# Performance work log

Measured on AMD Instinct MI355X. Metric: run time of the kernel, lower is better.

The kernel has to match this reference:

```python
import jax, jax.numpy as jnp
import numpy as np

N_NODES = 100000


def _gcn_layer(x, W, b, row, col, ew, n):
    # PyG GCNConv: x' = D^{-1/2} (A + I) D^{-1/2} (x W) + b
    xw = x @ W  # [N, out]
    deg = jax.ops.segment_sum(ew, col, num_segments=n)  # weighted in-degree incl. self loops
    dinv = jnp.where(deg > 0, jax.lax.rsqrt(deg), 0.0)
    norm = dinv[row] * ew * dinv[col]  # [E]
    msg = xw[row] * norm[:, None]  # [E, out] gather + scale
    out = jax.ops.segment_sum(msg, col, num_segments=n) + b
    return out


def setup_inputs() -> dict:
    key = jax.random.key(0)
    k = jax.random.split(key, 6)
    E = 1600000
    h = 64
    x = jax.random.normal(k[0], (N_NODES, 4), dtype=jnp.float32)
    edge_index = jax.random.randint(k[1], (2, E), 0, N_NODES, dtype=jnp.int64)
    edge_weight = jax.random.uniform(k[2], (E,), dtype=jnp.float32)
    W1 = jax.random.normal(k[3], (4, h), dtype=jnp.float32) * (1.0 / np.sqrt(4))
    b1 = jnp.zeros((h,), dtype=jnp.float32)
    W2 = jax.random.normal(k[4], (h, h), dtype=jnp.float32) * (1.0 / np.sqrt(h))
    b2 = jnp.zeros((h,), dtype=jnp.float32)
    return {"x": x, "edge_index": edge_index, "edge_weight": edge_weight,
            "W1": W1, "b1": b1, "W2": W2, "b2": b2}


def reference(x, edge_index, edge_weight, W1, b1, W2, b2):
    n = x.shape[0]
    # add self loops with weight 1 (GCNConv default add_self_loops=True)
    loop = jnp.arange(n, dtype=edge_index.dtype)
    row = jnp.concatenate([edge_index[0], loop])
    col = jnp.concatenate([edge_index[1], loop])
    ew = jnp.concatenate([edge_weight, jnp.ones((n,), dtype=edge_weight.dtype)])
    h = jax.nn.relu(_gcn_layer(x, W1, b1, row, col, ew, n))
    out = jax.nn.relu(_gcn_layer(h, W2, b2, row, col, ew, n))
    return out
```

## Files before the change

### kernel.cpp

```cpp
#include <hip/hip_runtime.h>

#define H 64
#define BKT_SHIFT 7
#define BKT_NODES 128
#define NB 782
#define CAP 2432
#define SC_K 8
#define SC_T 512
#define SC_TILE (SC_K * SC_T)

typedef __attribute__((ext_vector_type(8))) short short8v;
typedef __attribute__((ext_vector_type(4))) float float4v;

__device__ __forceinline__ float bf2f(unsigned short u) {
    return __uint_as_float(((unsigned)u) << 16);
}
__device__ __forceinline__ unsigned short f2bf(float f) {
    unsigned u = __float_as_uint(f);
    unsigned r = ((u >> 16) & 1u) + 0x7FFFu;
    return (unsigned short)((u + r) >> 16);
}
__device__ __forceinline__ float bflo(unsigned d) { return __uint_as_float(d << 16); }
__device__ __forceinline__ float bfhi(unsigned d) { return __uint_as_float(d & 0xFFFF0000u); }


__global__ void k_prep(const float* __restrict__ W2, unsigned short* __restrict__ W2Tb) {
    int g = blockIdx.x * 256 + threadIdx.x;
    if (g < H * H) {
        int c = g >> 6, k = g & 63;
        W2Tb[g] = f2bf(W2[k * H + c]);
    }
}


__global__ __launch_bounds__(SC_T) void k_bscatter(
        const int* __restrict__ row, const int* __restrict__ col,
        const float* __restrict__ ew, unsigned* __restrict__ cursor,
        uint2* __restrict__ sorted, int E) {
    __shared__ unsigned hist[NB];
    __shared__ unsigned gbase[NB];
    int t = threadIdx.x;
    for (int b = t; b < NB; b += SC_T) hist[b] = 0;
    __syncthreads();
    int tile = blockIdx.x * SC_TILE;
    unsigned st[SC_K];
#pragma unroll
    for (int k = 0; k < SC_K; ++k) {
        int e = tile + k * SC_T + t;
        unsigned enc = 0xFFFFFFFFu;
        if (e < E) {
            unsigned c = (unsigned)col[e];
            unsigned b = c >> BKT_SHIFT;
            unsigned nl = c & (BKT_NODES - 1);
            unsigned r = atomicAdd(&hist[b], 1u);
            enc = (b << 20) | (nl << 13) | r;
        }
        st[k] = enc;
    }
    __syncthreads();
    for (int b = t; b < NB; b += SC_T) {
        unsigned h = hist[b];
        if (h) gbase[b] = (unsigned)b * CAP + atomicAdd(&cursor[b], h);
    }
    __syncthreads();
#pragma unroll
    for (int k = 0; k < SC_K; ++k) {
        int e = tile + k * SC_T + t;
        if (e >= E) continue;
        unsigned enc = st[k];
        unsigned b = enc >> 20, nl = (enc >> 13) & 127u, r = enc & 8191u;
        unsigned pk = ((unsigned)row[e] << 7) | nl;
        sorted[gbase[b] + r] = make_uint2(pk, __float_as_uint(ew[e]));
    }
}


__global__ __launch_bounds__(256) void k_bsort(const uint2* __restrict__ sorted,
                                               const unsigned* __restrict__ cursor,
                                               const float* __restrict__ x,
                                               uint2* __restrict__ sorted2,
                                               unsigned* __restrict__ startA,
                                               unsigned* __restrict__ cntA,
                                               float* __restrict__ dinv,
                                               unsigned short* __restrict__ xqb, int n) {
    __shared__ unsigned hist[BKT_NODES];
    __shared__ unsigned base_[BKT_NODES];
    __shared__ float deg[BKT_NODES];
    __shared__ unsigned wsum;
    int b = blockIdx.x, t = threadIdx.x;
    if (t < BKT_NODES) { hist[t] = 0; deg[t] = 1.0f; }
    __syncthreads();
    unsigned s = (unsigned)b * CAP, e = s + cursor[b];
    uint2 st[10];
#pragma unroll
    for (int k = 0; k < 10; ++k) {
        unsigned j = s + (unsigned)t + ((unsigned)k << 8);
        if (j < e) {
            uint2 u = sorted[j];
            st[k] = u;
            unsigned nl = u.x & 127u;
            atomicAdd(&hist[nl], 1u);
            atomicAdd(&deg[nl], __uint_as_float(u.y));
        }
    }
    __syncthreads();
    if (t < BKT_NODES) {
        unsigned v = hist[t];
        unsigned sc = v;
#pragma unroll
        for (int d = 1; d < 64; d <<= 1) {
            unsigned u = __shfl_up(sc, d);
            if ((t & 63) >= d) sc += u;
        }
        if (t == 63) wsum = sc;
        base_[t] = sc - v;
        int node = b * BKT_NODES + t;
        if (node < n) {
            cntA[node] = v;
            float di = rsqrtf(deg[t]);
            dinv[node] = di;
            float4 xv = ((const float4*)x)[node];
            ushort4 o;
            o.x = f2bf(xv.x * di); o.y = f2bf(xv.y * di);
            o.z = f2bf(xv.z * di); o.w = f2bf(xv.w * di);
            ((ushort4*)xqb)[node] = o;
        }
        hist[t] = 0;
    }
    __syncthreads();
    if (t >= 64 && t < BKT_NODES) base_[t] += wsum;
    __syncthreads();
    if (t < BKT_NODES) {
        int node = b * BKT_NODES + t;
        if (node < n) startA[node] = s + base_[t];
    }
    __syncthreads();
#pragma unroll
    for (int k = 0; k < 10; ++k) {
        unsigned j = s + (unsigned)t + ((unsigned)k << 8);
        if (j < e) {
            uint2 u = st[k];
            unsigned nl = u.x & 127u;
            unsigned pos = atomicAdd(&hist[nl], 1u);
            sorted2[s + base_[nl] + pos] = make_uint2(u.x & 0xFFFFFF80u, u.y);
        }
    }
}


__global__ __launch_bounds__(256) void k_agg1(const uint2* __restrict__ sorted2,
                                              const unsigned* __restrict__ startA,
                                              const unsigned* __restrict__ cntA,
                                              const unsigned short* __restrict__ xqb,
                                              float4* __restrict__ agg4, int n) {
    int g = blockIdx.x * 256 + threadIdx.x;
    int node = g >> 1, half = g & 1;
    if (node >= n) return;
    unsigned s0 = startA[node];
    unsigned cnt = cntA[node];
    unsigned cH = cnt >> 1;
    unsigned s = s0 + (half ? cH : 0u);
    unsigned c = half ? (cnt - cH) : cH;
    const char* xq = (const char*)xqb;
    float a0, a1, a2, a3;
    if (half == 0) {
        uint2 sq = *(const uint2*)(xqb + ((size_t)node << 2));
        a0 = bflo(sq.x); a1 = bfhi(sq.x); a2 = bflo(sq.y); a3 = bfhi(sq.y);
    } else {
        a0 = a1 = a2 = a3 = 0.0f;
    }
    unsigned j = 0;
    for (; j + 8 <= c; j += 8) {
        uint2 p[8], q[8];
#pragma unroll
        for (int k = 0; k < 8; ++k) p[k] = sorted2[s + j + k];
#pragma unroll
        for (int k = 0; k < 8; ++k) q[k] = *(const uint2*)(xq + (p[k].x >> 4));
#pragma unroll
        for (int k = 0; k < 8; ++k) {
            float w = __uint_as_float(p[k].y);
            a0 = fmaf(bflo(q[k].x), w, a0); a1 = fmaf(bfhi(q[k].x), w, a1);
            a2 = fmaf(bflo(q[k].y), w, a2); a3 = fmaf(bfhi(q[k].y), w, a3);
        }
    }
    for (; j < c; ++j) {
        uint2 p = sorted2[s + j];
        uint2 q = *(const uint2*)(xq + (p.x >> 4));
        float w = __uint_as_float(p.y);
        a0 = fmaf(bflo(q.x), w, a0); a1 = fmaf(bfhi(q.x), w, a1);
        a2 = fmaf(bflo(q.y), w, a2); a3 = fmaf(bfhi(q.y), w, a3);
    }
    agg4[((size_t)node << 1) + half] = make_float4(a0, a1, a2, a3);
}


__global__ __launch_bounds__(256) void k_l2front(const float4* __restrict__ agg4,
                                                 const float* __restrict__ W1,
                                                 const float* __restrict__ b1,
                                                 const unsigned short* __restrict__ W2Tb,
                                                 const float* __restrict__ dinv,
                                                 unsigned short* __restrict__ xs2b, int n) {
    __shared__ unsigned short ht[64 * H];
    __shared__ unsigned short wt[H * H];
    __shared__ float w1s[4 * H];
    __shared__ float b1s[H];
    int tid = threadIdx.x;
    int base = blockIdx.x * 64;
    w1s[tid] = W1[tid];
    if (tid < H) b1s[tid] = b1[tid];
    for (int idx = tid; idx < 512; idx += 256) {
        int r = idx >> 3, c = idx & 7;
        uint4 v = *(const uint4*)(W2Tb + (r << 6) + (c << 3));
        *(uint4*)(wt + (r << 6) + ((c ^ (r & 7)) << 3)) = v;
    }
    __syncthreads();
    {
        int r = tid >> 2, ch = tid & 3;
        int node = base + r;
        float4 avA = (node < n) ? agg4[(size_t)node << 1] : make_float4(0.f, 0.f, 0.f, 0.f);
        float4 avB = (node < n) ? agg4[((size_t)node << 1) + 1] : make_float4(0.f, 0.f, 0.f, 0.f);
        float4 av = make_float4(avA.x + avB.x, avA.y + avB.y, avA.z + avB.z, avA.w + avB.w);
        float di = (node < n) ? dinv[node] : 0.0f;
#pragma unroll
        for (int cc = 0; cc < 2; ++cc) {
            int cl = ch * 2 + cc;
            uint4 ov;
            unsigned* op = (unsigned*)&ov;
#pragma unroll
            for (int d = 0; d < 4; ++d) {
                int col = (cl << 3) + (d << 1);
                float h0 = av.x * w1s[col]     + av.y * w1s[H + col]
                         + av.z * w1s[2*H+col] + av.w * w1s[3*H + col];
                float h1 = av.x * w1s[col+1]     + av.y * w1s[H + col+1]
                         + av.z * w1s[2*H+col+1] + av.w * w1s[3*H + col+1];
                h0 = fmaxf(di * h0 + b1s[col], 0.0f);
                h1 = fmaxf(di * h1 + b1s[col + 1], 0.0f);
                op[d] = ((unsigned)f2bf(h1) << 16) | f2bf(h0);
            }
            *(uint4*)(ht + (r << 6) + ((cl ^ (r & 7)) << 3)) = ov;
        }
    }
    __syncthreads();
    int lane = tid & 63;
    int wv = tid >> 6;
    int R = wv * 16;
    int lr = lane & 15, lq = lane >> 4;
    short8v a[2], b[4][2];
#pragma unroll
    for (int kk = 0; kk < 2; ++kk) {
        int rowi = R + lr;
        int cl = kk * 4 + lq;
        a[kk] = *(const short8v*)(ht + (rowi << 6) + ((cl ^ (rowi & 7)) << 3));
    }
#pragma unroll
    for (int nt = 0; nt < 4; ++nt)
#pragma unroll
        for (int kk = 0; kk < 2; ++kk) {
            int rowi = nt * 16 + lr;
            int cl = kk * 4 + lq;
            b[nt][kk] = *(const short8v*)(wt + (rowi << 6) + ((cl ^ (rowi & 7)) << 3));
        }
    float4v acc[4] = {};
#pragma unroll
    for (int nt = 0; nt < 4; ++nt)
#pragma unroll
        for (int kk = 0; kk < 2; ++kk)
            acc[nt] = __builtin_amdgcn_mfma_f32_16x16x32_bf16(a[kk], b[nt][kk],
                                                              acc[nt], 0, 0, 0);
#pragma unroll
    for (int i = 0; i < 4; ++i) {
        int node = base + R + lq * 4 + i;
        if (node < n) {
            float di = dinv[node];
#pragma unroll
            for (int nt = 0; nt < 4; ++nt)
                xs2b[((size_t)node << 6) + nt * 16 + lr] = f2bf(acc[nt][i] * di);
        }
    }
}


__global__ __launch_bounds__(256) void k_agg2(const uint2* __restrict__ sorted2,
                                              const unsigned* __restrict__ startA,
                                              const unsigned* __restrict__ cntA,
                                              const float* __restrict__ dinv,
                                              const unsigned short* __restrict__ xsb,
                                              const float* __restrict__ bias,
                                              float* __restrict__ outf, int n) {
    int wv = (int)(__builtin_amdgcn_readfirstlane(threadIdx.x) >> 6);
    int wid = blockIdx.x * 4 + wv;
    if (wid >= n) return;
    int lane = threadIdx.x & 63;
    int eg = lane >> 3;
    int c8 = lane & 7;
    unsigned s = startA[wid];
    unsigned cnt = cntA[wid];
    float di = dinv[wid];
    const char* xb = (const char*)xsb + (c8 << 4);
    float a0=0.f,a1=0.f,a2=0.f,a3=0.f,a4=0.f,a5=0.f,a6=0.f,a7=0.f;
    for (unsigned b = 0; b < cnt; b += 32) {
        unsigned iA = b + (unsigned)eg;
        unsigned iB = iA + 8u, iC = iA + 16u, iD = iA + 24u;
        uint2 pA = sorted2[s + (iA < cnt ? iA : 0u)];
        uint2 pB = sorted2[s + (iB < cnt ? iB : 0u)];
        uint2 pC = sorted2[s + (iC < cnt ? iC : 0u)];
        uint2 pD = sorted2[s + (iD < cnt ? iD : 0u)];
        float wA = iA < cnt ? __uint_as_float(pA.y) : 0.0f;
        float wB = iB < cnt ? __uint_as_float(pB.y) : 0.0f;
        float wC = iC < cnt ? __uint_as_float(pC.y) : 0.0f;
        float wD = iD < cnt ? __uint_as_float(pD.y) : 0.0f;
        uint4 dA = *(const uint4*)(xb + pA.x);
        uint4 dB = *(const uint4*)(xb + pB.x);
        uint4 dC = *(const uint4*)(xb + pC.x);
        uint4 dD = *(const uint4*)(xb + pD.x);
        a0 = fmaf(bflo(dA.x), wA, a0); a1 = fmaf(bfhi(dA.x), wA, a1);
        a2 = fmaf(bflo(dA.y), wA, a2); a3 = fmaf(bfhi(dA.y), wA, a3);
        a4 = fmaf(bflo(dA.z), wA, a4); a5 = fmaf(bfhi(dA.z), wA, a5);
        a6 = fmaf(bflo(dA.w), wA, a6); a7 = fmaf(bfhi(dA.w), wA, a7);
        a0 = fmaf(bflo(dB.x), wB, a0); a1 = fmaf(bfhi(dB.x), wB, a1);
        a2 = fmaf(bflo(dB.y), wB, a2); a3 = fmaf(bfhi(dB.y), wB, a3);
        a4 = fmaf(bflo(dB.z), wB, a4); a5 = fmaf(bfhi(dB.z), wB, a5);
        a6 = fmaf(bflo(dB.w), wB, a6); a7 = fmaf(bfhi(dB.w), wB, a7);
        a0 = fmaf(bflo(dC.x), wC, a0); a1 = fmaf(bfhi(dC.x), wC, a1);
        a2 = fmaf(bflo(dC.y), wC, a2); a3 = fmaf(bfhi(dC.y), wC, a3);
        a4 = fmaf(bflo(dC.z), wC, a4); a5 = fmaf(bfhi(dC.z), wC, a5);
        a6 = fmaf(bflo(dC.w), wC, a6); a7 = fmaf(bfhi(dC.w), wC, a7);
        a0 = fmaf(bflo(dD.x), wD, a0); a1 = fmaf(bfhi(dD.x), wD, a1);
        a2 = fmaf(bflo(dD.y), wD, a2); a3 = fmaf(bfhi(dD.y), wD, a3);
        a4 = fmaf(bflo(dD.z), wD, a4); a5 = fmaf(bfhi(dD.z), wD, a5);
        a6 = fmaf(bflo(dD.w), wD, a6); a7 = fmaf(bfhi(dD.w), wD, a7);
    }
    a0 += __shfl_xor(a0, 8); a0 += __shfl_xor(a0, 16); a0 += __shfl_xor(a0, 32);
    a1 += __shfl_xor(a1, 8); a1 += __shfl_xor(a1, 16); a1 += __shfl_xor(a1, 32);
    a2 += __shfl_xor(a2, 8); a2 += __shfl_xor(a2, 16); a2 += __shfl_xor(a2, 32);
    a3 += __shfl_xor(a3, 8); a3 += __shfl_xor(a3, 16); a3 += __shfl_xor(a3, 32);
    a4 += __shfl_xor(a4, 8); a4 += __shfl_xor(a4, 16); a4 += __shfl_xor(a4, 32);
    a5 += __shfl_xor(a5, 8); a5 += __shfl_xor(a5, 16); a5 += __shfl_xor(a5, 32);
    a6 += __shfl_xor(a6, 8); a6 += __shfl_xor(a6, 16); a6 += __shfl_xor(a6, 32);
    a7 += __shfl_xor(a7, 8); a7 += __shfl_xor(a7, 16); a7 += __shfl_xor(a7, 32);
    uint4 sv = *(const uint4*)((const char*)xsb + (((size_t)(unsigned)wid) << 7) + (c8 << 4));
    a0 += bflo(sv.x); a1 += bfhi(sv.x);
    a2 += bflo(sv.y); a3 += bfhi(sv.y);
    a4 += bflo(sv.z); a5 += bfhi(sv.z);
    a6 += bflo(sv.w); a7 += bfhi(sv.w);
    const float* bp = bias + (c8 << 3);
    float r0 = fmaxf(di * a0 + bp[0], 0.0f);
    float r1 = fmaxf(di * a1 + bp[1], 0.0f);
    float r2 = fmaxf(di * a2 + bp[2], 0.0f);
    float r3 = fmaxf(di * a3 + bp[3], 0.0f);
    float r4 = fmaxf(di * a4 + bp[4], 0.0f);
    float r5 = fmaxf(di * a5 + bp[5], 0.0f);
    float r6 = fmaxf(di * a6 + bp[6], 0.0f);
    float r7 = fmaxf(di * a7 + bp[7], 0.0f);
    if (eg == 0) {
        float4 o = {r0, r1, r2, r3};
        *(float4*)(outf + (((size_t)wid) << 6) + (c8 << 3)) = o;
    } else if (eg == 1) {
        float4 o = {r4, r5, r6, r7};
        *(float4*)(outf + (((size_t)wid) << 6) + (c8 << 3) + 4) = o;
    }
}


extern "C" void kernel_launch(void* const* d_in, const int* in_sizes, int n_in,
                              void* d_out, int out_size, void* d_ws, size_t ws_size,
                              hipStream_t stream) {
    const float* x  = (const float*)d_in[0];
    const int*   ei = (const int*)d_in[1];
    const float* ew = (const float*)d_in[2];
    const float* W1 = (const float*)d_in[3];
    const float* b1 = (const float*)d_in[4];
    const float* W2 = (const float*)d_in[5];
    const float* b2 = (const float*)d_in[6];
    float* out = (float*)d_out;

    const int n = in_sizes[0] / 4;
    const int E = in_sizes[2];
    const int* row = ei;
    const int* col = ei + E;

    char* p = (char*)d_ws;
    unsigned* cursor = (unsigned*)p;            p += 1024 * 4;
    unsigned short* W2Tb = (unsigned short*)p;  p += (size_t)H * H * 2;
    float* dinv      = (float*)p;               p += (size_t)n * 4;
    unsigned* startA = (unsigned*)p;            p += (size_t)n * 4;
    unsigned* cntA   = (unsigned*)p;            p += (size_t)n * 4;
    unsigned short* xqb = (unsigned short*)p;   p += (size_t)n * 4 * 2;
    float4* agg4     = (float4*)p;              p += ((size_t)2 * n + 128) * 16;
    unsigned short* xs2b = (unsigned short*)p;  p += ((size_t)n + 1) * H * 2;
    uint2* sorted    = (uint2*)p;               p += ((size_t)NB * CAP + 64) * 8;
    uint2* sorted2   = (uint2*)p;

    (void)hipMemsetAsync(cursor, 0, 1024 * 4, stream);
    k_prep<<<16, 256, 0, stream>>>(W2, W2Tb);

    k_bscatter<<<(E + SC_TILE - 1) / SC_TILE, SC_T, 0, stream>>>(row, col, ew, cursor, sorted, E);

    k_bsort<<<NB, 256, 0, stream>>>(sorted, cursor, x, sorted2, startA, cntA, dinv, xqb, n);

    k_agg1<<<(2 * n + 255) / 256, 256, 0, stream>>>(sorted2, startA, cntA, xqb, agg4, n);

    k_l2front<<<(n + 63) / 64, 256, 0, stream>>>(agg4, W1, b1, W2Tb, dinv, xs2b, n);

    k_agg2<<<(n + 3) / 4, 256, 0, stream>>>(sorted2, startA, cntA, dinv, xs2b, b2, out, n);
}
```

Before: 125.1 us.

## Split edge bucket scatter into two-pass coarse then fine radix binning

Replaces the single-pass scatter into 782 buckets with two passes. The first pass bins edges into 49 coarse buckets and stores the 4-bit fine bucket id in the low mantissa bits of the edge weight. The second pass splits each coarse bucket into 16 fine buckets. The aim is better write coalescing and fewer global atomics, since each block writes into fewer destinations. The cost is an extra read and write of the edge array, and the weight's low 4 mantissa bits are overwritten, which slightly perturbs precision.

```diff
diff --git a/kernel.cpp b/kernel.cpp
--- a/kernel.cpp
+++ b/kernel.cpp
@@ -5,9 +5,10 @@
 #define BKT_NODES 128
 #define NB 782
 #define CAP 2432
-#define SC_K 8
-#define SC_T 512
-#define SC_TILE (SC_K * SC_T)
+#define NC 49
+#define CAPC 38400
+#define NCHUNK 5
+#define CHB (CAPC / NCHUNK)
 
 typedef __attribute__((ext_vector_type(8))) short short8v;
 typedef __attribute__((ext_vector_type(4))) float float4v;
@@ -33,44 +34,97 @@
 }
 
 
-__global__ __launch_bounds__(SC_T) void k_bscatter(
+__global__ __launch_bounds__(512) void k_binA(
         const int* __restrict__ row, const int* __restrict__ col,
-        const float* __restrict__ ew, unsigned* __restrict__ cursor,
-        uint2* __restrict__ sorted, int E) {
-    __shared__ unsigned hist[NB];
-    __shared__ unsigned gbase[NB];
+        const float* __restrict__ ew, unsigned* __restrict__ cursorC,
+        uint2* __restrict__ coarse, int E) {
+    __shared__ unsigned hist[NC];
+    __shared__ unsigned gbase[NC];
     int t = threadIdx.x;
-    for (int b = t; b < NB; b += SC_T) hist[b] = 0;
-    __syncthreads();
-    int tile = blockIdx.x * SC_TILE;
-    unsigned st[SC_K];
-#pragma unroll
-    for (int k = 0; k < SC_K; ++k) {
-        int e = tile + k * SC_T + t;
+    if (t < NC) hist[t] = 0;
+    __syncthreads();
+    int tile = blockIdx.x * 8192;
+    unsigned st[16];
+#pragma unroll
+    for (int k = 0; k < 16; ++k) {
+        int e = tile + k * 512 + t;
         unsigned enc = 0xFFFFFFFFu;
         if (e < E) {
             unsigned c = (unsigned)col[e];
-            unsigned b = c >> BKT_SHIFT;
-            unsigned nl = c & (BKT_NODES - 1);
-            unsigned r = atomicAdd(&hist[b], 1u);
-            enc = (b << 20) | (nl << 13) | r;
+            unsigned cb = c >> 11;
+            unsigned fl = (c >> 7) & 15u;
+            unsigned nl = c & 127u;
+            unsigned r = atomicAdd(&hist[cb], 1u);
+            enc = (cb << 24) | (fl << 20) | (nl << 13) | r;
         }
         st[k] = enc;
     }
     __syncthreads();
-    for (int b = t; b < NB; b += SC_T) {
-        unsigned h = hist[b];
-        if (h) gbase[b] = (unsigned)b * CAP + atomicAdd(&cursor[b], h);
-    }
-    __syncthreads();
-#pragma unroll
-    for (int k = 0; k < SC_K; ++k) {
-        int e = tile + k * SC_T + t;
+    if (t < NC) {
+        unsigned h = hist[t];
+        if (h) gbase[t] = (unsigned)t * CAPC + atomicAdd(&cursorC[t], h);
+    }
+    __syncthreads();
+#pragma unroll
+    for (int k = 0; k < 16; ++k) {
+        int e = tile + k * 512 + t;
         if (e >= E) continue;
         unsigned enc = st[k];
-        unsigned b = enc >> 20, nl = (enc >> 13) & 127u, r = enc & 8191u;
+        unsigned cb = enc >> 24, fl = (enc >> 20) & 15u;
+        unsigned nl = (enc >> 13) & 127u, r = enc & 8191u;
         unsigned pk = ((unsigned)row[e] << 7) | nl;
-        sorted[gbase[b] + r] = make_uint2(pk, __float_as_uint(ew[e]));
+        unsigned wb = (__float_as_uint(ew[e]) & 0xFFFFFFF0u) | fl;
+        coarse[gbase[cb] + r] = make_uint2(pk, wb);
+    }
+}
+
+
+__global__ __launch_bounds__(512) void k_binB(
+        const uint2* __restrict__ coarse, const unsigned* __restrict__ cursorC,
+        unsigned* __restrict__ cursorF, uint2* __restrict__ sorted) {
+    __shared__ unsigned hist4[4][16];
+    __shared__ unsigned gbase4[4][16];
+    int t = threadIdx.x;
+    int c = blockIdx.x / NCHUNK;
+    int ch = blockIdx.x % NCHUNK;
+    int grp = t >> 7;
+    if (t < 64) ((unsigned*)hist4)[t] = 0;
+    __syncthreads();
+    int cntC = (int)cursorC[c];
+    int base0 = c * CAPC + ch * CHB;
+    int m = cntC - ch * CHB; if (m > CHB) m = CHB; if (m < 0) m = 0;
+    unsigned st[15];
+#pragma unroll
+    for (int k = 0; k < 15; ++k) {
+        int i = t + k * 512;
+        unsigned enc = 0xFFFFFFFFu;
+        if (i < m) {
+            unsigned fl = coarse[base0 + i].y & 15u;
+            unsigned r = atomicAdd(&hist4[grp][fl], 1u);
+            enc = (fl << 13) | r;
+        }
+        st[k] = enc;
+    }
+    __syncthreads();
+    if (t < 16) {
+        unsigned h0 = hist4[0][t], h1 = hist4[1][t], h2 = hist4[2][t], h3 = hist4[3][t];
+        unsigned tot = h0 + h1 + h2 + h3;
+        int fb = c * 16 + t;
+        unsigned gb = 0;
+        if (tot) gb = (unsigned)fb * CAP + atomicAdd(&cursorF[fb], tot);
+        gbase4[0][t] = gb;
+        gbase4[1][t] = gb + h0;
+        gbase4[2][t] = gb + h0 + h1;
+        gbase4[3][t] = gb + h0 + h1 + h2;
+    }
+    __syncthreads();
+#pragma unroll
+    for (int k = 0; k < 15; ++k) {
+        int i = t + k * 512;
+        if (i >= m) continue;
+        unsigned enc = st[k];
+        unsigned fl = (enc >> 13) & 15u, r = enc & 8191u;
+        sorted[gbase4[grp][fl] + r] = coarse[base0 + i];
     }
 }
 
@@ -390,13 +444,18 @@
     unsigned short* xs2b = (unsigned short*)p;  p += ((size_t)n + 1) * H * 2;
     uint2* sorted    = (uint2*)p;               p += ((size_t)NB * CAP + 64) * 8;
     uint2* sorted2   = (uint2*)p;
+    uint2* coarse    = sorted2;
+    unsigned* cursorC = cursor + 800;
+    unsigned* cursorF = cursor;
 
     (void)hipMemsetAsync(cursor, 0, 1024 * 4, stream);
     k_prep<<<16, 256, 0, stream>>>(W2, W2Tb);
 
-    k_bscatter<<<(E + SC_TILE - 1) / SC_TILE, SC_T, 0, stream>>>(row, col, ew, cursor, sorted, E);
-
-    k_bsort<<<NB, 256, 0, stream>>>(sorted, cursor, x, sorted2, startA, cntA, dinv, xqb, n);
+    k_binA<<<(E + 8191) / 8192, 512, 0, stream>>>(row, col, ew, cursorC, coarse, E);
+
+    k_binB<<<NC * NCHUNK, 512, 0, stream>>>(coarse, cursorC, cursorF, sorted);
+
+    k_bsort<<<NB, 256, 0, stream>>>(sorted, cursorF, x, sorted2, startA, cntA, dinv, xqb, n);
 
     k_agg1<<<(2 * n + 255) / 256, 256, 0, stream>>>(sorted2, startA, cntA, xqb, agg4, n);
 
```

Measured after the change: 130.1 us. 1.04x slower.
